# Optimization experiments

Measured on AMD Instinct MI355X. Metric: run time of the kernel, lower is better.

## Reference

```python
import jax, jax.numpy as jnp
import numpy as np

ITER = 6
GAMMA = 0.99
Q = 0.95


def _maxpool(x, win, stride, pad):
    # NCHW max pool
    return jax.lax.reduce_window(
        x, -jnp.inf, jax.lax.max,
        (1, 1, win, win), (1, 1, stride, stride),
        ((0, 0), (0, 0), (pad, pad), (pad, pad)))


def _nearest(x, size):
    # torch F.interpolate(mode='nearest'): src = floor(dst * in / out)
    H, W = size
    h_in, w_in = x.shape[2], x.shape[3]
    ih = (jnp.arange(H) * h_in) // H
    iw = (jnp.arange(W) * w_in) // W
    return x[:, :, ih[:, None], iw[None, :]]


def setup_inputs() -> dict:
    key = jax.random.key(0)
    ks = jax.random.split(key, 4)
    C, mid = 256, 16  # mid = int(sqrt(C))
    x = jax.random.normal(ks[0], (16, C, 128, 128), jnp.float32)
    w1 = jax.random.normal(ks[1], (mid, C), jnp.float32) / np.sqrt(C)
    b1 = jnp.zeros((mid,), jnp.float32)
    w2 = jax.random.normal(ks[2], (C, mid), jnp.float32) / np.sqrt(mid)
    b2 = jnp.zeros((C,), jnp.float32)
    return {"x": x, "w1": w1, "b1": b1, "w2": w2, "b2": b2}


def reference(x, w1, b1, w2, b2):
    B, C, H, W = x.shape
    # --- quantile activation mask (detached) ---
    flat = x.reshape(B, C, H * W)
    thr = jnp.quantile(flat, Q, axis=-1)[:, :, None, None]  # [B,C,1,1]
    M = jax.lax.stop_gradient((x >= thr).astype(x.dtype))
    # --- propagate field ---
    feat = x * M
    out = feat
    for i in range(ITER):
        g = jnp.asarray(GAMMA ** (2 ** i), x.dtype)
        if i == 0:
            feat = _maxpool(feat, 3, 1, 1) * g  # same-resolution 3x3 pool
            out = jnp.maximum(out, feat)
        else:
            # 5x5 stride-2 pool -> scale -> nearest upsample back to (H,W)
            feat = _nearest(_maxpool(feat, 5, 2, 2) * g, (H, W))
            out = jnp.maximum(out, feat)
    # --- receptor modulator: 1x1 conv -> relu -> 1x1 conv -> sigmoid ---
    h = jax.nn.relu(jnp.einsum('bchw,mc->bmhw', out, w1) + b1[None, :, None, None])
    R = jax.nn.sigmoid(jnp.einsum('bmhw,cm->bchw', h, w2) + b2[None, :, None, None])
    y = x * R
    return y
```

## Files before the change

### kernel.cpp

```cpp
#include <hip/hip_runtime.h>
#include <cmath>
#include <cfloat>

#define HW_ 16384

__device__ __forceinline__ unsigned f2key(float f){
    unsigned u = __float_as_uint(f);
    return u ^ ((u & 0x80000000u) ? 0xFFFFFFFFu : 0x80000000u);
}
__device__ __forceinline__ float key2f(unsigned k){
    unsigned u = (k & 0x80000000u) ? (k ^ 0x80000000u) : ~k;
    return __uint_as_float(u);
}
__device__ __forceinline__ float bf2f(unsigned short s){
    return __uint_as_float((unsigned)s << 16);
}
__device__ __forceinline__ unsigned pkmax(unsigned a, unsigned b){
    unsigned d;
    asm("v_pk_max_u16 %0, %1, %2" : "=v"(d) : "v"(a), "v"(b));
    return d;
}
__device__ __forceinline__ unsigned alignb(unsigned hi, unsigned lo){
    unsigned d;
    asm("v_alignbit_b32 %0, %1, %2, 16" : "=v"(d) : "v"(hi), "v"(lo));
    return d;
}
__device__ __forceinline__ unsigned cvtpk(float lo, float hi){
    unsigned d;
    asm("v_cvt_pk_bf16_f32 %0, %1, %2" : "=v"(d) : "v"(lo), "v"(hi));
    return d;
}
__device__ __forceinline__ unsigned wscan_incl(unsigned v, int lane){
    #pragma unroll
    for (int o = 1; o < 64; o <<= 1){
        unsigned u = __shfl_up(v, o);
        v += (lane >= o) ? u : 0u;
    }
    return v;
}

__global__ __launch_bounds__(512, 6) void k1f(
    const float* __restrict__ x,
    unsigned short* __restrict__ outp, unsigned short* __restrict__ m64g,
    float g1, float q2, float q3, float q4, float q5, float q6)
{
    __shared__ __align__(16) unsigned short C0[16384];
    __shared__ __align__(16) unsigned short H5s[8192];
    __shared__ unsigned hist[1024];
    __shared__ unsigned wsum[8];
    __shared__ unsigned redA[8], redB[8];
    __shared__ unsigned s_dA, s_dB, s_cloA, s_cloB, s_keyA, s_keyB;

    const int tid = threadIdx.x;
    const int lane = tid & 63;
    const int wid = tid >> 6;
    const unsigned bc = blockIdx.x;
    const float4* xp4 = (const float4*)(x + (size_t)bc * HW_);

    unsigned key[32];

    #pragma unroll
    for (int k = 0; k < 2; ++k) hist[tid + k * 512] = 0u;
    __syncthreads();
    #pragma unroll
    for (int k = 0; k < 8; ++k){
        float4 v = xp4[tid + k * 512];
        key[4*k+0] = f2key(v.x);
        key[4*k+1] = f2key(v.y);
        key[4*k+2] = f2key(v.z);
        key[4*k+3] = f2key(v.w);
        atomicAdd(&hist[key[4*k+0] >> 22], 1u);
        atomicAdd(&hist[key[4*k+1] >> 22], 1u);
        atomicAdd(&hist[key[4*k+2] >> 22], 1u);
        atomicAdd(&hist[key[4*k+3] >> 22], 1u);
    }
    __syncthreads();

    unsigned rA = 15563u, rB = 15564u;
    unsigned prefVal = 0u, prefMask = 0u;
    bool done = false;

    {
        unsigned part = hist[tid*2] + hist[tid*2+1];
        unsigned incl = wscan_incl(part, lane);
        if (lane == 63) wsum[wid] = incl;
        __syncthreads();
        unsigned off = 0;
        #pragma unroll
        for (int w = 0; w < 8; ++w) off += (w < wid) ? wsum[w] : 0u;
        unsigned phi = incl + off;
        unsigned plo = phi - part;
        if (rA >= plo && rA < phi){
            unsigned c = plo;
            #pragma unroll
            for (int k = 0; k < 2; ++k){
                unsigned hh = hist[tid*2+k];
                if (rA < c + hh){ s_dA = tid*2+k; s_cloA = c; break; }
                c += hh;
            }
        }
        if (rB >= plo && rB < phi){
            unsigned c = plo;
            #pragma unroll
            for (int k = 0; k < 2; ++k){
                unsigned hh = hist[tid*2+k];
                if (rB < c + hh){ s_dB = tid*2+k; s_cloB = c; break; }
                c += hh;
            }
        }
        __syncthreads();
        unsigned dA = s_dA, dB = s_dB;
        if (dA != dB){
            unsigned locA = 0u, locB = 0xFFFFFFFFu;
            #pragma unroll
            for (int e = 0; e < 32; ++e){
                unsigned d = key[e] >> 22;
                if (d == dA) locA = max(locA, key[e]);
                if (d == dB) locB = min(locB, key[e]);
            }
            #pragma unroll
            for (int o = 32; o > 0; o >>= 1){
                locA = max(locA, __shfl_down(locA, o));
                locB = min(locB, __shfl_down(locB, o));
            }
            if (lane == 0){ redA[wid] = locA; redB[wid] = locB; }
            __syncthreads();
            if (tid == 0){
                unsigned a = redA[0], b = redB[0];
                for (int w = 1; w < 8; ++w){ a = max(a, redA[w]); b = min(b, redB[w]); }
                s_keyA = a; s_keyB = b;
            }
            __syncthreads();
            done = true;
        } else {
            prefVal = dA << 22; prefMask = 0x3FFu << 22;
            rA -= s_cloA; rB -= s_cloB;
            __syncthreads();
        }
    }

    if (!done){
        const int shifts[3] = {14, 6, 0};
        const int bitsv[3]  = {8, 8, 6};
        for (int lvl = 0; lvl < 3 && !done; ++lvl){
            int shift = shifts[lvl];
            unsigned nb = 1u << bitsv[lvl];
            unsigned msk = nb - 1u;
            if (tid < (int)nb) hist[tid] = 0u;
            __syncthreads();
            #pragma unroll
            for (int e = 0; e < 32; ++e){
                if ((key[e] & prefMask) == prefVal)
                    atomicAdd(&hist[(key[e] >> shift) & msk], 1u);
            }
            __syncthreads();
            unsigned part = (tid < (int)nb) ? hist[tid] : 0u;
            unsigned incl = wscan_incl(part, lane);
            if (lane == 63) wsum[wid] = incl;
            __syncthreads();
            unsigned off = 0;
            #pragma unroll
            for (int w = 0; w < 8; ++w) off += (w < wid) ? wsum[w] : 0u;
            unsigned phi = incl + off;
            unsigned plo = phi - part;
            if (tid < (int)nb){
                if (rA >= plo && rA < phi){ s_dA = tid; s_cloA = plo; }
                if (rB >= plo && rB < phi){ s_dB = tid; s_cloB = plo; }
            }
            __syncthreads();
            unsigned dA = s_dA, dB = s_dB;
            if (dA != dB){
                unsigned mA = prefMask | (msk << shift);
                unsigned vAp = prefVal | (dA << shift);
                unsigned vBp = prefVal | (dB << shift);
                unsigned locA = 0u, locB = 0xFFFFFFFFu;
                #pragma unroll
                for (int e = 0; e < 32; ++e){
                    if ((key[e] & mA) == vAp) locA = max(locA, key[e]);
                    if ((key[e] & mA) == vBp) locB = min(locB, key[e]);
                }
                #pragma unroll
                for (int o = 32; o > 0; o >>= 1){
                    locA = max(locA, __shfl_down(locA, o));
                    locB = min(locB, __shfl_down(locB, o));
                }
                if (lane == 0){ redA[wid] = locA; redB[wid] = locB; }
                __syncthreads();
                if (tid == 0){
                    unsigned a = redA[0], b = redB[0];
                    for (int w = 1; w < 8; ++w){ a = max(a, redA[w]); b = min(b, redB[w]); }
                    s_keyA = a; s_keyB = b;
                }
                __syncthreads();
                done = true;
            } else {
                prefVal |= dA << shift;
                prefMask |= msk << shift;
                rA -= s_cloA; rB -= s_cloB;
                if (lvl == 2){
                    if (tid == 0){ s_keyA = prefVal; s_keyB = prefVal; }
                    done = true;
                }
                __syncthreads();
            }
        }
    }

    float vlo = key2f(s_keyA);
    float vhi = key2f(s_keyB);
    float idxq = 0.95f * 16383.0f;
    float frac = idxq - floorf(idxq);
    const float thr = vlo * (1.0f - frac) + vhi * frac;

    #pragma unroll
    for (int k = 0; k < 8; ++k){
        int i = tid + k * 512;
        float f0 = key2f(key[4*k+0]); f0 = (f0 >= thr) ? f0 : 0.0f;
        float f1 = key2f(key[4*k+1]); f1 = (f1 >= thr) ? f1 : 0.0f;
        float f2 = key2f(key[4*k+2]); f2 = (f2 >= thr) ? f2 : 0.0f;
        float f3 = key2f(key[4*k+3]); f3 = (f3 >= thr) ? f3 : 0.0f;
        uint2 w; w.x = cvtpk(f0, f1); w.y = cvtpk(f2, f3);
        ((uint2*)C0)[i] = w;
    }
    __syncthreads();

    {
        const unsigned* C0w = (const unsigned*)C0;
        unsigned* outp32 = (unsigned*)(outp + (size_t)bc * HW_);
        const int wc = lane;
        const int r0 = wid * 16;

        unsigned hmA, hmB, hmC, cA, cB, cC;
        {
            int r = r0 - 1;
            if (r < 0){ hmA = 0u; cA = 0u; }
            else {
                unsigned w = C0w[r*64 + wc];
                unsigned wl = __shfl_up(w, 1);
                unsigned wr = __shfl_down(w, 1);
                if (wc == 0)  wl = 0u;
                if (wc == 63) wr = 0u;
                hmA = pkmax(pkmax(alignb(w, wl), w), alignb(wr, w));
                cA = w;
            }
        }
        {
            int r = r0;
            unsigned w = C0w[r*64 + wc];
            unsigned wl = __shfl_up(w, 1);
            unsigned wr = __shfl_down(w, 1);
            if (wc == 0)  wl = 0u;
            if (wc == 63) wr = 0u;
            hmB = pkmax(pkmax(alignb(w, wl), w), alignb(wr, w));
            cB = w;
        }
        #pragma unroll
        for (int rr = 0; rr < 16; ++rr){
            int r = r0 + rr;
            {
                int rn = r + 1;
                if (rn > 127){ hmC = 0u; cC = 0u; }
                else {
                    unsigned w = C0w[rn*64 + wc];
                    unsigned wl = __shfl_up(w, 1);
                    unsigned wr = __shfl_down(w, 1);
                    if (wc == 0)  wl = 0u;
                    if (wc == 63) wr = 0u;
                    hmC = pkmax(pkmax(alignb(w, wl), w), alignb(wr, w));
                    cC = w;
                }
            }
            unsigned p1 = pkmax(pkmax(hmA, hmB), hmC);
            float a0 = g1 * bf2f((unsigned short)(p1 & 0xFFFFu));
            float a1v = g1 * bf2f((unsigned short)(p1 >> 16));
            outp32[r*64 + wc] = pkmax(cB, cvtpk(a0, a1v));
            unsigned wjm1 = __shfl_up(p1, 1);
            unsigned wjp1 = __shfl_down(p1, 1);
            if (wc == 0)  wjm1 = 0u;
            if (wc == 63) wjp1 = 0u;
            unsigned s = pkmax(wjm1, p1);
            s = pkmax(s, s >> 16);
            s = pkmax(s, wjp1 & 0xFFFFu);
            H5s[r*64 + wc] = (unsigned short)s;
            hmA = hmB; hmB = hmC; cB = cC;
        }
    }
    __syncthreads();

    unsigned* U = (unsigned*)C0;
    unsigned* T = ((unsigned*)C0) + 2048;
    float mf[8];
    #pragma unroll
    for (int k = 0; k < 4; ++k){
        int q = tid + k * 512;
        int i = q >> 5, wj = q & 31;
        int rr = 2 * i;
        const unsigned* H5w = (const unsigned*)H5s;
        unsigned m = pkmax(H5w[rr*32 + wj], H5w[(rr+1)*32 + wj]);
        if (rr >= 1) m = pkmax(m, H5w[(rr-1)*32 + wj]);
        if (rr >= 2) m = pkmax(m, H5w[(rr-2)*32 + wj]);
        if (rr + 2 <= 127) m = pkmax(m, H5w[(rr+2)*32 + wj]);
        U[q] = m;
        mf[2*k]   = q2 * bf2f((unsigned short)(m & 0xFFFFu));
        mf[2*k+1] = q2 * bf2f((unsigned short)(m >> 16));
    }
    __syncthreads();

    const float gs[4] = {q3, q4, q5, q6};
    #pragma unroll
    for (int it = 0; it < 4; ++it){
        #pragma unroll
        for (int k = 0; k < 4; ++k){
            int q = tid + k * 512;
            unsigned w = U[q];
            unsigned wl = __shfl_up(w, 1);
            unsigned wr = __shfl_down(w, 1);
            if ((q & 31) == 0)  wl = 0u;
            if ((q & 31) == 31) wr = 0u;
            T[q] = pkmax(pkmax(alignb(w, wl), w), alignb(wr, w));
        }
        __syncthreads();
        #pragma unroll
        for (int k = 0; k < 4; ++k){
            int q = tid + k * 512;
            int r = q >> 5;
            unsigned w = T[q];
            if (r > 0)  w = pkmax(w, T[q - 32]);
            if (r < 63) w = pkmax(w, T[q + 32]);
            U[q] = w;
            mf[2*k]   = fmaxf(mf[2*k],   gs[it] * bf2f((unsigned short)(w & 0xFFFFu)));
            mf[2*k+1] = fmaxf(mf[2*k+1], gs[it] * bf2f((unsigned short)(w >> 16)));
        }
        __syncthreads();
    }

    {
        unsigned* mp = (unsigned*)(m64g + (size_t)bc * 4096);
        #pragma unroll
        for (int k = 0; k < 4; ++k){
            int q = tid + k * 512;
            mp[q] = cvtpk(mf[2*k], mf[2*k+1]);
        }
    }
}

__global__ __launch_bounds__(256) void k3_mlp(
    const float* __restrict__ x, const unsigned short* __restrict__ outp,
    const unsigned short* __restrict__ m64,
    const float* __restrict__ w1, const float* __restrict__ b1,
    const float* __restrict__ w2, const float* __restrict__ b2,
    float* __restrict__ y)
{
    __shared__ __align__(16) float W1s[256 * 16];
    __shared__ __align__(16) float W2s[256 * 16];
    __shared__ float B1s[16];
    __shared__ float B2s[256];
    const int tid = threadIdx.x;
    const int blk = blockIdx.x;
    const int b = blk >> 6;
    const int t = blk & 63;

    for (int q = tid; q < 4096; q += 256){
        int c = q >> 4, m = q & 15;
        W1s[q] = w1[m * 256 + c];
        W2s[q] = w2[q];
    }
    if (tid < 16) B1s[tid] = b1[tid];
    B2s[tid] = b2[tid];
    __syncthreads();

    const int pix = t * 256 + tid;
    const int mi = (pix >> 8) * 64 + ((pix & 127) >> 1);
    const size_t base = (size_t)b * 256 * HW_;
    const size_t mbase = (size_t)b * 256 * 4096;

    float h[16];
    #pragma unroll
    for (int m = 0; m < 16; ++m) h[m] = 0.0f;

    #pragma unroll 4
    for (int c = 0; c < 256; ++c){
        float o  = bf2f(outp[base + (size_t)c * HW_ + pix]);
        float mo = bf2f(m64[mbase + (size_t)c * 4096 + mi]);
        o = fmaxf(o, mo);
        const float4* wr = (const float4*)&W1s[c * 16];
        float4 a0 = wr[0], a1 = wr[1], a2 = wr[2], a3 = wr[3];
        h[0]  = fmaf(a0.x, o, h[0]);  h[1]  = fmaf(a0.y, o, h[1]);
        h[2]  = fmaf(a0.z, o, h[2]);  h[3]  = fmaf(a0.w, o, h[3]);
        h[4]  = fmaf(a1.x, o, h[4]);  h[5]  = fmaf(a1.y, o, h[5]);
        h[6]  = fmaf(a1.z, o, h[6]);  h[7]  = fmaf(a1.w, o, h[7]);
        h[8]  = fmaf(a2.x, o, h[8]);  h[9]  = fmaf(a2.y, o, h[9]);
        h[10] = fmaf(a2.z, o, h[10]); h[11] = fmaf(a2.w, o, h[11]);
        h[12] = fmaf(a3.x, o, h[12]); h[13] = fmaf(a3.y, o, h[13]);
        h[14] = fmaf(a3.z, o, h[14]); h[15] = fmaf(a3.w, o, h[15]);
    }
    #pragma unroll
    for (int m = 0; m < 16; ++m) h[m] = fmaxf(h[m] + B1s[m], 0.0f);

    #pragma unroll 4
    for (int c = 0; c < 256; ++c){
        const float4* wr = (const float4*)&W2s[c * 16];
        float4 a0 = wr[0], a1 = wr[1], a2 = wr[2], a3 = wr[3];
        float acc = B2s[c];
        acc += a0.x * h[0]  + a0.y * h[1]  + a0.z * h[2]  + a0.w * h[3];
        acc += a1.x * h[4]  + a1.y * h[5]  + a1.z * h[6]  + a1.w * h[7];
        acc += a2.x * h[8]  + a2.y * h[9]  + a2.z * h[10] + a2.w * h[11];
        acc += a3.x * h[12] + a3.y * h[13] + a3.z * h[14] + a3.w * h[15];
        float R = 1.0f / (1.0f + __expf(-acc));
        float xv = x[base + (size_t)c * HW_ + pix];
        y[base + (size_t)c * HW_ + pix] = xv * R;
    }
}

extern "C" void kernel_launch(void* const* d_in, const int* in_sizes, int n_in,
                              void* d_out, int out_size, void* d_ws, size_t ws_size,
                              hipStream_t stream) {
    const float* x  = (const float*)d_in[0];
    const float* w1 = (const float*)d_in[1];
    const float* b1 = (const float*)d_in[2];
    const float* w2 = (const float*)d_in[3];
    const float* b2 = (const float*)d_in[4];
    float* y  = (float*)d_out;
    char* ws = (char*)d_ws;

    unsigned short* outp = (unsigned short*)ws;
    unsigned short* m64  = (unsigned short*)(ws + 134217728);

    float g1 = 0.99f;
    float q2 = (float)std::pow(0.99, 3.0);
    float q3 = (float)std::pow(0.99, 7.0);
    float q4 = (float)std::pow(0.99, 15.0);
    float q5 = (float)std::pow(0.99, 31.0);
    float q6 = (float)std::pow(0.99, 63.0);

    k1f<<<4096, 512, 0, stream>>>(x, outp, m64, g1, q2, q3, q4, q5, q6);
    k3_mlp<<<1024, 256, 0, stream>>>(x, outp, m64, w1, b1, w2, b2, y);
}
```

Measured before the change: 314.6 us.

## Use bf16 MFMA with hi/lo weight split for the 1x1 conv MLP

Replaces the scalar FMA per-pixel MLP kernel with one that stages a 64-pixel tile of the pooled field in swizzled LDS and runs both 1x1 convolutions on 16x16x32 bf16 MFMA. Weights and hidden activations are split into bf16 hi/lo parts to keep accuracy close to fp32. The grid grows to 4096 blocks of 64 pixels each. This targets the VALU cost of the 256x16 and 16x256 FMA chains, in exchange for extra staging, bf16 rounding error and smaller per-block tiles. It also drops an unused register in k1f.

```diff
diff --git a/kernel.cpp b/kernel.cpp
--- a/kernel.cpp
+++ b/kernel.cpp
@@ -11,6 +11,11 @@
 __device__ __forceinline__ float key2f(unsigned k){
     unsigned u = (k & 0x80000000u) ? (k ^ 0x80000000u) : ~k;
     return __uint_as_float(u);
+}
+__device__ __forceinline__ unsigned short f2bf(float f){
+    unsigned u = __float_as_uint(f);
+    unsigned r = u + 0x7FFFu + ((u >> 16) & 1u);
+    return (unsigned short)(r >> 16);
 }
 __device__ __forceinline__ float bf2f(unsigned short s){
     return __uint_as_float((unsigned)s << 16);
@@ -37,6 +42,12 @@
         v += (lane >= o) ? u : 0u;
     }
     return v;
+}
+
+typedef short bf16x8 __attribute__((ext_vector_type(8)));
+typedef float f32x4  __attribute__((ext_vector_type(4)));
+__device__ __forceinline__ bf16x8 tofrag(uint4 q){
+    union { uint4 q; bf16x8 f; } u; u.q = q; return u.f;
 }
 
 __global__ __launch_bounds__(512, 6) void k1f(
@@ -230,10 +241,10 @@
         const int wc = lane;
         const int r0 = wid * 16;
 
-        unsigned hmA, hmB, hmC, cA, cB, cC;
+        unsigned hmA, hmB, hmC, cB, cC;
         {
             int r = r0 - 1;
-            if (r < 0){ hmA = 0u; cA = 0u; }
+            if (r < 0){ hmA = 0u; }
             else {
                 unsigned w = C0w[r*64 + wc];
                 unsigned wl = __shfl_up(w, 1);
@@ -241,7 +252,6 @@
                 if (wc == 0)  wl = 0u;
                 if (wc == 63) wr = 0u;
                 hmA = pkmax(pkmax(alignb(w, wl), w), alignb(wr, w));
-                cA = w;
             }
         }
         {
@@ -344,71 +354,118 @@
     }
 }
 
-__global__ __launch_bounds__(256) void k3_mlp(
+__global__ __launch_bounds__(256) void k3_mfma(
     const float* __restrict__ x, const unsigned short* __restrict__ outp,
     const unsigned short* __restrict__ m64,
     const float* __restrict__ w1, const float* __restrict__ b1,
     const float* __restrict__ w2, const float* __restrict__ b2,
     float* __restrict__ y)
 {
-    __shared__ __align__(16) float W1s[256 * 16];
-    __shared__ __align__(16) float W2s[256 * 16];
-    __shared__ float B1s[16];
-    __shared__ float B2s[256];
-    const int tid = threadIdx.x;
-    const int blk = blockIdx.x;
-    const int b = blk >> 6;
-    const int t = blk & 63;
-
-    for (int q = tid; q < 4096; q += 256){
-        int c = q >> 4, m = q & 15;
-        W1s[q] = w1[m * 256 + c];
-        W2s[q] = w2[q];
-    }
-    if (tid < 16) B1s[tid] = b1[tid];
-    B2s[tid] = b2[tid];
-    __syncthreads();
-
-    const int pix = t * 256 + tid;
-    const int mi = (pix >> 8) * 64 + ((pix & 127) >> 1);
-    const size_t base = (size_t)b * 256 * HW_;
-    const size_t mbase = (size_t)b * 256 * 4096;
-
-    float h[16];
-    #pragma unroll
-    for (int m = 0; m < 16; ++m) h[m] = 0.0f;
+    __shared__ __align__(16) unsigned short SOUT[16384];
+    __shared__ __align__(16) unsigned short W1h[16*264];
+    __shared__ __align__(16) unsigned short W1l[16*264];
+    __shared__ __align__(16) unsigned short W2s[256*40];
+    __shared__ __align__(16) float HS[4*16*18];
+
+    const int tid  = threadIdx.x;
+    const int lane = tid & 63;
+    const int wid  = tid >> 6;
+    const int blk  = blockIdx.x;
+    const int b    = blk >> 8;
+    const int px0  = (blk & 255) * 64;
+
+    for (int e = tid; e < 4096; e += 256){
+        int m = e >> 8, c = e & 255;
+        float f = w1[m*256 + c];
+        unsigned short hi = f2bf(f);
+        W1h[m*264 + c] = hi;
+        W1l[m*264 + c] = f2bf(f - bf2f(hi));
+    }
+    for (int e = tid; e < 4096; e += 256){
+        int c = e >> 4, m = e & 15;
+        float f = w2[e];
+        unsigned short hi = f2bf(f);
+        W2s[c*40 + m]      = hi;
+        W2s[c*40 + 16 + m] = f2bf(f - bf2f(hi));
+    }
+    {
+        const int row = px0 >> 7;
+        const int mibase = (row >> 1)*64 + ((px0 & 127) >> 1);
+        const unsigned* op32 = (const unsigned*)(outp + (size_t)b*256*HW_);
+        const unsigned short* mp = m64 + (size_t)b*256*4096;
+        #pragma unroll
+        for (int i = 0; i < 32; ++i){
+            int u = tid + i*256;
+            int ch = u >> 5, pxp = u & 31;
+            unsigned o2 = op32[(ch*HW_ + px0)/2 + pxp];
+            unsigned short mv = mp[ch*4096 + mibase + pxp];
+            unsigned v = pkmax(o2, (unsigned)mv * 0x10001u);
+            int pa = 2*pxp, pb = pa + 1;
+            SOUT[(pa*512 + ((ch*2) ^ ((pa & 30) << 3))) >> 1] = (unsigned short)v;
+            SOUT[(pb*512 + ((ch*2) ^ ((pb & 30) << 3))) >> 1] = (unsigned short)(v >> 16);
+        }
+    }
+    __syncthreads();
+
+    const int nidx = lane & 15;
+    const int kg   = lane >> 4;
+    const int px_t = wid*16 + nidx;
+
+    f32x4 acc = {0.f, 0.f, 0.f, 0.f};
+    #pragma unroll
+    for (int ks = 0; ks < 8; ++ks){
+        int byteB = px_t*512 + ((ks*64 + kg*16) ^ ((px_t & 30) << 3));
+        uint4 qb = *(const uint4*)((const char*)SOUT + byteB);
+        bf16x8 fb = tofrag(qb);
+        int byteA = nidx*528 + ks*64 + kg*16;
+        uint4 qh = *(const uint4*)((const char*)W1h + byteA);
+        uint4 ql = *(const uint4*)((const char*)W1l + byteA);
+        acc = __builtin_amdgcn_mfma_f32_16x16x32_bf16(tofrag(qh), fb, acc, 0, 0, 0);
+        acc = __builtin_amdgcn_mfma_f32_16x16x32_bf16(tofrag(ql), fb, acc, 0, 0, 0);
+    }
+    #pragma unroll
+    for (int i2 = 0; i2 < 4; ++i2){
+        int mid = kg*4 + i2;
+        float hv = fmaxf(acc[i2] + b1[mid], 0.0f);
+        HS[(wid*16 + nidx)*18 + mid] = hv;
+    }
+    __syncthreads();
+
+    bf16x8 bh = {0,0,0,0,0,0,0,0}, bl = {0,0,0,0,0,0,0,0};
+    if (kg < 2){
+        const float* hp = &HS[(wid*16 + nidx)*18 + kg*8];
+        float f0 = hp[0], f1 = hp[1], f2 = hp[2], f3 = hp[3];
+        float f4 = hp[4], f5 = hp[5], f6 = hp[6], f7 = hp[7];
+        unsigned short h0 = f2bf(f0), h1 = f2bf(f1), h2 = f2bf(f2), h3 = f2bf(f3);
+        unsigned short h4 = f2bf(f4), h5 = f2bf(f5), h6 = f2bf(f6), h7 = f2bf(f7);
+        bh[0] = (short)h0; bh[1] = (short)h1; bh[2] = (short)h2; bh[3] = (short)h3;
+        bh[4] = (short)h4; bh[5] = (short)h5; bh[6] = (short)h6; bh[7] = (short)h7;
+        bl[0] = (short)f2bf(f0 - bf2f(h0)); bl[1] = (short)f2bf(f1 - bf2f(h1));
+        bl[2] = (short)f2bf(f2 - bf2f(h2)); bl[3] = (short)f2bf(f3 - bf2f(h3));
+        bl[4] = (short)f2bf(f4 - bf2f(h4)); bl[5] = (short)f2bf(f5 - bf2f(h5));
+        bl[6] = (short)f2bf(f6 - bf2f(h6)); bl[7] = (short)f2bf(f7 - bf2f(h7));
+    }
 
     #pragma unroll 4
-    for (int c = 0; c < 256; ++c){
-        float o  = bf2f(outp[base + (size_t)c * HW_ + pix]);
-        float mo = bf2f(m64[mbase + (size_t)c * 4096 + mi]);
-        o = fmaxf(o, mo);
-        const float4* wr = (const float4*)&W1s[c * 16];
-        float4 a0 = wr[0], a1 = wr[1], a2 = wr[2], a3 = wr[3];
-        h[0]  = fmaf(a0.x, o, h[0]);  h[1]  = fmaf(a0.y, o, h[1]);
-        h[2]  = fmaf(a0.z, o, h[2]);  h[3]  = fmaf(a0.w, o, h[3]);
-        h[4]  = fmaf(a1.x, o, h[4]);  h[5]  = fmaf(a1.y, o, h[5]);
-        h[6]  = fmaf(a1.z, o, h[6]);  h[7]  = fmaf(a1.w, o, h[7]);
-        h[8]  = fmaf(a2.x, o, h[8]);  h[9]  = fmaf(a2.y, o, h[9]);
-        h[10] = fmaf(a2.z, o, h[10]); h[11] = fmaf(a2.w, o, h[11]);
-        h[12] = fmaf(a3.x, o, h[12]); h[13] = fmaf(a3.y, o, h[13]);
-        h[14] = fmaf(a3.z, o, h[14]); h[15] = fmaf(a3.w, o, h[15]);
-    }
-    #pragma unroll
-    for (int m = 0; m < 16; ++m) h[m] = fmaxf(h[m] + B1s[m], 0.0f);
-
-    #pragma unroll 4
-    for (int c = 0; c < 256; ++c){
-        const float4* wr = (const float4*)&W2s[c * 16];
-        float4 a0 = wr[0], a1 = wr[1], a2 = wr[2], a3 = wr[3];
-        float acc = B2s[c];
-        acc += a0.x * h[0]  + a0.y * h[1]  + a0.z * h[2]  + a0.w * h[3];
-        acc += a1.x * h[4]  + a1.y * h[5]  + a1.z * h[6]  + a1.w * h[7];
-        acc += a2.x * h[8]  + a2.y * h[9]  + a2.z * h[10] + a2.w * h[11];
-        acc += a3.x * h[12] + a3.y * h[13] + a3.z * h[14] + a3.w * h[15];
-        float R = 1.0f / (1.0f + __expf(-acc));
-        float xv = x[base + (size_t)c * HW_ + pix];
-        y[base + (size_t)c * HW_ + pix] = xv * R;
+    for (int t = 0; t < 16; ++t){
+        bf16x8 a2h = {0,0,0,0,0,0,0,0}, a2l = {0,0,0,0,0,0,0,0};
+        if (kg < 2){
+            const char* basep = (const char*)W2s + (t*16 + nidx)*80;
+            a2h = tofrag(*(const uint4*)(basep + kg*16));
+            a2l = tofrag(*(const uint4*)(basep + 32 + kg*16));
+        }
+        f32x4 d2 = {0.f, 0.f, 0.f, 0.f};
+        d2 = __builtin_amdgcn_mfma_f32_16x16x32_bf16(a2h, bh, d2, 0, 0, 0);
+        d2 = __builtin_amdgcn_mfma_f32_16x16x32_bf16(a2l, bh, d2, 0, 0, 0);
+        d2 = __builtin_amdgcn_mfma_f32_16x16x32_bf16(a2h, bl, d2, 0, 0, 0);
+        #pragma unroll
+        for (int i2 = 0; i2 < 4; ++i2){
+            int ch = t*16 + kg*4 + i2;
+            float logit = d2[i2] + b2[ch];
+            float R = 1.0f / (1.0f + __expf(-logit));
+            size_t gidx = ((size_t)(b*256 + ch))*HW_ + px0 + px_t;
+            y[gidx] = x[gidx] * R;
+        }
     }
 }
 
@@ -434,5 +491,5 @@
     float q6 = (float)std::pow(0.99, 63.0);
 
     k1f<<<4096, 512, 0, stream>>>(x, outp, m64, g1, q2, q3, q4, q5, q6);
-    k3_mlp<<<1024, 256, 0, stream>>>(x, outp, m64, w1, b1, w2, b2, y);
-}
+    k3_mfma<<<4096, 256, 0, stream>>>(x, outp, m64, w1, b1, w2, b2, y);
+}
```

Result: slower. 349.3 us (+11.0%).
